# Kernel tuning notes

Hardware: AMD Instinct MI355X
Metric: run time of the kernel (lower is better)

The kernel has to match this reference:

```python
import jax, jax.numpy as jnp
import numpy as np

N_BINS = 64
INPUT_DIM = 8
R = 1.2
BOUND = 10.0
BETA = 1e-06
N = 2097152


def _mesh_and_elmt():
    m = N_BINS / 2
    idx = jnp.arange(N_BINS + 1, dtype=jnp.float32) - m
    x1L = BOUND * (R - 1.0) / (R ** m - 1.0)
    xr = (1.0 - R ** jnp.abs(idx)) / (1.0 - R)
    xr = jnp.where(idx >= 0, x1L * xr, -x1L * xr)
    xr = (xr + BOUND) / (2.0 * BOUND)
    mesh = jnp.concatenate([jnp.zeros((1,), jnp.float32), xr[1:-1], jnp.ones((1,), jnp.float32)])  # [n_bins+1]
    elmt = mesh[1:] - mesh[:-1]  # [n_bins]
    return mesh, elmt


def _pdf_normalize(p, elmt):
    # pdf: [n_bins+1, d]; F_ref: [n_bins, d] cumulative bin integrals
    p0 = jnp.full((1, INPUT_DIM), BETA, jnp.float32)
    ep = jnp.exp(p)
    px = ep * ((elmt[:-1] + elmt[1:]) / 2.0)[:, None]
    scale = (1.0 - (elmt[0] + elmt[-1]) * BETA / 2.0) / jnp.sum(px, 0, keepdims=True)
    px = scale * ep
    pdf = jnp.concatenate([p0, px, p0], 0)
    cell = (pdf[:-1] + pdf[1:]) / 2.0 * elmt[:, None]  # [n_bins, d]
    F_ref = jnp.concatenate([jnp.zeros((1, INPUT_DIM), jnp.float32),
                             jnp.cumsum(cell, 0)[:N_BINS - 1]], 0)
    return pdf, F_ref


def setup_inputs() -> dict:
    key = jax.random.key(0)
    k1, k2 = jax.random.split(key)
    x = jax.random.normal(k1, (N, INPUT_DIM), dtype=jnp.float32)
    logdet = jnp.zeros((N, 1), dtype=jnp.float32)
    p = jax.random.normal(k2, (N_BINS - 1, INPUT_DIM), dtype=jnp.float32)
    return {"x": x, "logdet": logdet, "p": p}


def reference(x, logdet, p):
    mesh, elmt = _mesh_and_elmt()
    pdf, F_ref = _pdf_normalize(p, elmt)

    xs = (x + BOUND) / (2.0 * BOUND)  # [N, d] in [0,1] for covered points
    k = jnp.searchsorted(mesh, xs, side='right') - 1  # [N, d]
    cover = (k >= 0) & (k <= N_BINS - 1)
    k = jnp.clip(k, 0, N_BINS - 1)
    col = jnp.arange(INPUT_DIM)[None, :]

    v1 = pdf[k, col]            # [N, d]
    v2 = pdf[k + 1, col]
    xm = xs - mesh[k]
    h = elmt[k]
    F_pre = F_ref[k, col]

    y = jnp.where(cover, F_pre + xm * xm / 2.0 * (v2 - v1) / h + xm * v1, xs)
    dld = jnp.where(cover, xm * (v2 - v1) / h + v1, 1.0)
    logdet = logdet + jnp.sum(jnp.log(dld), -1, keepdims=True)

    y = y * 2.0 * BOUND - BOUND
    y = jnp.where(y > BOUND, BETA * (y - BOUND) + BOUND, y)
    logdet = logdet + jnp.sum(jnp.log(jnp.where(y > BOUND, BETA, 1.0)), -1, keepdims=True)
    y = jnp.where(y < -BOUND, BETA * (y + BOUND) - BOUND, y)
    logdet = logdet + jnp.sum(jnp.log(jnp.where(y < -BOUND, BETA, 1.0)), -1, keepdims=True)
    return y, logdet
```

## Files before the change

### kernel.cpp

```cpp
#include <hip/hip_runtime.h>
#include <math.h>

#define NDIM   8
#define NBINS  64
#define LOG_BETA   (-13.815510557964274f)
#define LN2F       0.69314718055994531f
#define ALPHA      34.0821892f
#define INV_LOG2R  3.80178401692393f
#define L2R        0.26303440583379378f

typedef float f32x4 __attribute__((ext_vector_type(4)));

__global__ __launch_bounds__(256, 8) void cdfq_fused(const float* __restrict__ x,
                                                     const float* __restrict__ logdet_in,
                                                     const float* __restrict__ p,
                                                     float* __restrict__ y_out,
                                                     float* __restrict__ ld_out,
                                                     int n)
{
    __shared__ float4 stbl[NDIM * NBINS];

    const int t  = threadIdx.x;
    const int T  = gridDim.x * blockDim.x;
    const int i0 = blockIdx.x * blockDim.x + t;
    const int G  = 2 * n;
    const int iters = G / T;
    const float4* xv4 = (const float4*)x;

    float4 X0, X1, X2; float L0, L1, Lc2;
    if (iters > 0) { X0 = xv4[i0];         L0  = logdet_in[i0 >> 1]; }
    if (iters > 1) { X1 = xv4[i0 + T];     L1  = logdet_in[(i0 + T) >> 1]; }
    if (iters > 2) { X2 = xv4[i0 + 2 * T]; Lc2 = logdet_in[(i0 + 2 * T) >> 1]; }
    __builtin_amdgcn_sched_barrier(0);

    {
        const int lane = t & 63;
        const int w    = t >> 6;
        const float pw32 = exp2f(32.0f * L2R);
        const float inv  = 0.5f / (pw32 - 1.0f);
        auto meshf = [&](float tt) {
            float fidx = tt - 32.0f;
            float pw = exp2f(fabsf(fidx) * L2R);
            float r  = (pw - 1.0f) * inv;
            return 0.5f + ((fidx >= 0.0f) ? r : -r);
        };
        const float m0  = meshf((float)lane);
        const float m1  = meshf((float)(lane + 1));
        const float el  = m1 - m0;
        const float el1 = __shfl_down(el, 1);
        const float e0e63 = 2.0f * (meshf(1.0f) - meshf(0.0f));

#pragma unroll
        for (int dd = 0; dd < 2; ++dd) {
            const int d = 2 * w + dd;
            float ep = 0.0f;
            if (lane < 63) ep = __expf(p[lane * NDIM + d]);
            float s = ep * 0.5f * (el + el1);
#pragma unroll
            for (int off = 32; off; off >>= 1) s += __shfl_xor(s, off);
            const float scale = (1.0f - e0e63 * 5e-7f) / s;
            const float epu = __shfl_up(ep, 1);
            const float pdl = (lane == 0)  ? 1e-6f : scale * epu;
            const float pdn = (lane == 63) ? 1e-6f : scale * ep;
            const float cell = 0.5f * (pdl + pdn) * el;
            float v = cell;
#pragma unroll
            for (int off = 1; off < 64; off <<= 1) {
                float u = __shfl_up(v, off);
                if (lane >= off) v += u;
            }
            stbl[(d << 6) | lane] = make_float4(pdl, (pdn - pdl) / el, v - cell, m0);
        }
    }
    __syncthreads();

    const float4* tbl = &stbl[((i0 & 1) << 2) << 6];
    const bool evenlane = ((i0 & 1) == 0);

    auto body = [&](float4 Xv, float Lin, int g) {
        float xd[4] = {Xv.x, Xv.y, Xv.z, Xv.w};
        float yd[4], dd4[4];
        float extra = 0.0f;

#pragma unroll
        for (int dl = 0; dl < 4; ++dl) {
            float xo = xd[dl];
            float u  = fabsf(xo);
            float xs = fmaf(xo, 0.05f, 0.5f);
            float gg = __log2f(fmaf(ALPHA, u, 1.0f)) * INV_LOG2R;
            int jf = (int)fminf(gg, 31.0f);
            int k  = ((xo >= 0.0f) ? 32 : 31) ^ jf;

            float4 tb = tbl[(dl << 6) + k];
            float xm  = xs - tb.w;
            bool cov  = (u < 10.0f);

            float yc = fmaf(xm, fmaf(0.5f * xm, tb.y, tb.x), tb.z);
            float dv = fmaf(xm, tb.y, tb.x);
            float yy = cov ? yc : xs;
            dd4[dl]  = cov ? dv : 1.0f;

            yy = fmaf(yy, 20.0f, -10.0f);
            if (yy > 10.0f)  { yy = fmaf(1e-6f, yy - 10.0f, 10.0f);  extra += LOG_BETA; }
            if (yy < -10.0f) { yy = fmaf(1e-6f, yy + 10.0f, -10.0f); extra += LOG_BETA; }
            yd[dl] = yy;
        }

        float l2 = __log2f(dd4[0] * dd4[1]) + __log2f(dd4[2] * dd4[3]);
        float contrib = fmaf(l2, LN2F, extra);
        float cross   = __shfl_xor(contrib, 1);

        f32x4 yv = { yd[0], yd[1], yd[2], yd[3] };
        __builtin_nontemporal_store(yv, (f32x4*)y_out + g);
        if (evenlane)
            __builtin_nontemporal_store(Lin + contrib + cross, ld_out + (g >> 1));
    };

    for (int j = 0; j < iters; ++j) {
        float4 Xn; float Ln;
        const bool more = (j + 3 < iters);
        if (more) {
            int gx = i0 + (j + 3) * T;
            Xn = xv4[gx];
            Ln = logdet_in[gx >> 1];
        }
        __builtin_amdgcn_sched_barrier(0);

        body(X0, L0, i0 + j * T);

        X0 = X1; L0 = L1;
        X1 = X2; L1 = Lc2;
        if (more) { X2 = Xn; Lc2 = Ln; }
    }

    int gr = i0 + iters * T;
    if (gr < G) {
        body(xv4[gr], logdet_in[gr >> 1], gr);
    }
}

extern "C" void kernel_launch(void* const* d_in, const int* in_sizes, int n_in,
                              void* d_out, int out_size, void* d_ws, size_t ws_size,
                              hipStream_t stream) {
    const float* x      = (const float*)d_in[0];
    const float* logdet = (const float*)d_in[1];
    const float* p      = (const float*)d_in[2];

    const int n = in_sizes[1];
    float* y_out  = (float*)d_out;
    float* ld_out = (float*)d_out + (size_t)n * NDIM;

    const int block = 256;
    int grid = 2048;
    if ((long long)grid * block > 2LL * n) grid = (2 * n + block - 1) / block;
    cdfq_fused<<<grid, block, 0, stream>>>(x, logdet, p, y_out, ld_out, n);
}
```

Before: 135.2 us.

## Unroll main loop by two and split LDS gathers from compute

Restructures the grid-stride loop to process two elements per iteration. It issues all LDS table gathers for both elements before consuming them, so LDS latency can overlap. The prefetch depth changes from a three-deep register rotation to prefetching the next pair. Occupancy hint drops from 8 to 7 waves, which gives more registers at the cost of fewer resident waves.

Result: no change. 135.7 us (+0.4%).

```diff
diff --git a/kernel.cpp b/kernel.cpp
--- a/kernel.cpp
+++ b/kernel.cpp
@@ -11,7 +11,7 @@
 
 typedef float f32x4 __attribute__((ext_vector_type(4)));
 
-__global__ __launch_bounds__(256, 8) void cdfq_fused(const float* __restrict__ x,
+__global__ __launch_bounds__(256, 7) void cdfq_fused(const float* __restrict__ x,
                                                      const float* __restrict__ logdet_in,
                                                      const float* __restrict__ p,
                                                      float* __restrict__ y_out,
@@ -25,12 +25,11 @@
     const int i0 = blockIdx.x * blockDim.x + t;
     const int G  = 2 * n;
     const int iters = G / T;
-    const float4* xv4 = (const float4*)x;
+    const f32x4* xv4 = (const f32x4*)x;
 
-    float4 X0, X1, X2; float L0, L1, Lc2;
-    if (iters > 0) { X0 = xv4[i0];         L0  = logdet_in[i0 >> 1]; }
-    if (iters > 1) { X1 = xv4[i0 + T];     L1  = logdet_in[(i0 + T) >> 1]; }
-    if (iters > 2) { X2 = xv4[i0 + 2 * T]; Lc2 = logdet_in[(i0 + 2 * T) >> 1]; }
+    f32x4 X0, X1; float L0, L1;
+    if (iters > 0) { X0 = xv4[i0];     L0 = logdet_in[i0 >> 1]; }
+    if (iters > 1) { X1 = xv4[i0 + T]; L1 = logdet_in[(i0 + T) >> 1]; }
     __builtin_amdgcn_sched_barrier(0);
 
     {
@@ -77,26 +76,30 @@
     const float4* tbl = &stbl[((i0 & 1) << 2) << 6];
     const bool evenlane = ((i0 & 1) == 0);
 
-    auto body = [&](float4 Xv, float Lin, int g) {
-        float xd[4] = {Xv.x, Xv.y, Xv.z, Xv.w};
+    auto gatherA = [&](f32x4 Xv, f32x4* tb) {
+#pragma unroll
+        for (int dl = 0; dl < 4; ++dl) {
+            float xo = Xv[dl];
+            float gg = __log2f(fmaf(ALPHA, fabsf(xo), 1.0f)) * INV_LOG2R;
+            int jf = (int)fminf(gg, 31.0f);
+            int k  = ((xo >= 0.0f) ? 32 : 31) ^ jf;
+            tb[dl] = *(const f32x4*)&tbl[(dl << 6) + k];
+        }
+    };
+
+    auto consumeB = [&](f32x4 Xv, const f32x4* tb, float Lin, int g) {
         float yd[4], dd4[4];
         float extra = 0.0f;
-
 #pragma unroll
         for (int dl = 0; dl < 4; ++dl) {
-            float xo = xd[dl];
-            float u  = fabsf(xo);
+            float xo = Xv[dl];
             float xs = fmaf(xo, 0.05f, 0.5f);
-            float gg = __log2f(fmaf(ALPHA, u, 1.0f)) * INV_LOG2R;
-            int jf = (int)fminf(gg, 31.0f);
-            int k  = ((xo >= 0.0f) ? 32 : 31) ^ jf;
+            f32x4 tv = tb[dl];
+            float xm = xs - tv[3];
+            bool cov = (fabsf(xo) < 10.0f);
 
-            float4 tb = tbl[(dl << 6) + k];
-            float xm  = xs - tb.w;
-            bool cov  = (u < 10.0f);
-
-            float yc = fmaf(xm, fmaf(0.5f * xm, tb.y, tb.x), tb.z);
-            float dv = fmaf(xm, tb.y, tb.x);
+            float yc = fmaf(xm, fmaf(0.5f * xm, tv[1], tv[0]), tv[2]);
+            float dv = fmaf(xm, tv[1], tv[0]);
             float yy = cov ? yc : xs;
             dd4[dl]  = cov ? dv : 1.0f;
 
@@ -105,7 +108,6 @@
             if (yy < -10.0f) { yy = fmaf(1e-6f, yy + 10.0f, -10.0f); extra += LOG_BETA; }
             yd[dl] = yy;
         }
-
         float l2 = __log2f(dd4[0] * dd4[1]) + __log2f(dd4[2] * dd4[3]);
         float contrib = fmaf(l2, LN2F, extra);
         float cross   = __shfl_xor(contrib, 1);
@@ -116,26 +118,34 @@
             __builtin_nontemporal_store(Lin + contrib + cross, ld_out + (g >> 1));
     };
 
-    for (int j = 0; j < iters; ++j) {
-        float4 Xn; float Ln;
-        const bool more = (j + 3 < iters);
-        if (more) {
-            int gx = i0 + (j + 3) * T;
-            Xn = xv4[gx];
-            Ln = logdet_in[gx >> 1];
-        }
+    int j = 0;
+    for (; j + 1 < iters; j += 2) {
+        f32x4 X2, X3; float L2, L3;
+        const bool m2 = (j + 2 < iters), m3 = (j + 3 < iters);
+        if (m2) { X2 = xv4[i0 + (j + 2) * T]; L2 = logdet_in[(i0 + (j + 2) * T) >> 1]; }
+        if (m3) { X3 = xv4[i0 + (j + 3) * T]; L3 = logdet_in[(i0 + (j + 3) * T) >> 1]; }
         __builtin_amdgcn_sched_barrier(0);
 
-        body(X0, L0, i0 + j * T);
+        f32x4 tb0[4], tb1[4];
+        gatherA(X0, tb0);
+        gatherA(X1, tb1);
+        consumeB(X0, tb0, L0, i0 + j * T);
+        consumeB(X1, tb1, L1, i0 + (j + 1) * T);
 
+        if (m2) { X0 = X2; L0 = L2; }
+        if (m3) { X1 = X3; L1 = L3; }
+    }
+    for (; j < iters; ++j) {
+        f32x4 tb0[4];
+        gatherA(X0, tb0);
+        consumeB(X0, tb0, L0, i0 + j * T);
         X0 = X1; L0 = L1;
-        X1 = X2; L1 = Lc2;
-        if (more) { X2 = Xn; Lc2 = Ln; }
     }
-
-    int gr = i0 + iters * T;
-    if (gr < G) {
-        body(xv4[gr], logdet_in[gr >> 1], gr);
+    for (int g = i0 + iters * T; g < G; g += T) {
+        f32x4 Xr = xv4[g]; float Lr = logdet_in[g >> 1];
+        f32x4 tbr[4];
+        gatherA(Xr, tbr);
+        consumeB(Xr, tbr, Lr, g);
     }
 }
 
```
